# Kernel optimization log

Measured on AMD Instinct MI355X. Metric: run time of the kernel, lower is better.

Reference implementation:

```python
import jax, jax.numpy as jnp
import numpy as np

# ---- model dims (match init_kwargs) ----
B, C, T = 64, 128, 512          # batch, n_channel, n_tokens
H = 256                          # n_hidden
GRID_SIZE = 5
SPLINE_ORDER = 3
N_COEFF = GRID_SIZE + SPLINE_ORDER   # 8 basis functions per input feature
GRID_RANGE = (-1.0, 1.0)
LN_EPS = 1e-5


def make_grid(in_features):
    # efficient-KAN extended knot grid: (in_features, grid_size + 2*order + 1)
    h = (GRID_RANGE[1] - GRID_RANGE[0]) / GRID_SIZE
    g = jnp.arange(-SPLINE_ORDER, GRID_SIZE + SPLINE_ORDER + 1, dtype=jnp.float32) * h + GRID_RANGE[0]
    return jnp.broadcast_to(g, (in_features, g.shape[0]))


def b_splines(x, grid):
    # x: (N, in), grid: (in, G+2k+1) -> (N, in, G+k) via Cox-de Boor recursion
    xg = x[:, :, None]
    bases = ((xg >= grid[:, :-1]) & (xg < grid[:, 1:])).astype(x.dtype)
    for k in range(1, SPLINE_ORDER + 1):
        left = (xg - grid[:, : -(k + 1)]) / (grid[:, k:-1] - grid[:, : -(k + 1)])
        right = (grid[:, k + 1:] - xg) / (grid[:, k + 1:] - grid[:, 1:-k])
        bases = left * bases[:, :, :-1] + right * bases[:, :, 1:]
    return bases


def kan_linear(x, grid, base_w, spline_w, spline_scaler):
    # x: (..., in) -> (..., out). base: silu(x)@W^T, plus spline combination.
    lead = x.shape[:-1]
    x2 = x.reshape(-1, x.shape[-1])
    base_out = jax.nn.silu(x2) @ base_w.T                              # (N, out)
    sw = spline_w * spline_scaler[:, :, None]                          # (out, in, coeff)
    spl_out = jnp.einsum('nic,oic->no', b_splines(x2, grid), sw)       # (N, out)
    return (base_out + spl_out).reshape(*lead, base_w.shape[0])


def setup_inputs() -> dict:
    key = jax.random.key(0)
    ks = jax.random.split(key, 8)
    scale1 = 1.0 / np.sqrt(C)
    scale2 = 1.0 / np.sqrt(H)
    return {
        "U": jax.random.normal(ks[0], (B, C, T), dtype=jnp.float32),
        "ln_w": jnp.ones((T, C), dtype=jnp.float32),
        "ln_b": jnp.zeros((T, C), dtype=jnp.float32),
        "bw1": jax.random.normal(ks[1], (H, C), dtype=jnp.float32) * scale1,
        "sw1": jax.random.normal(ks[2], (H, C, N_COEFF), dtype=jnp.float32) * (0.1 * scale1),
        "ss1": jnp.ones((H, C), dtype=jnp.float32),
        "bw2": jax.random.normal(ks[3], (C, H), dtype=jnp.float32) * scale2,
        "sw2": jax.random.normal(ks[4], (C, H, N_COEFF), dtype=jnp.float32) * (0.1 * scale2),
        "ss2": jnp.ones((C, H), dtype=jnp.float32),
    }


def reference(U, ln_w, ln_b, bw1, sw1, ss1, bw2, sw2, ss2):
    g1 = make_grid(C)
    g2 = make_grid(H)
    z = jnp.transpose(U, (0, 2, 1))                                   # (B, T, C)
    mu = jnp.mean(z, axis=(-2, -1), keepdims=True)
    var = jnp.var(z, axis=(-2, -1), keepdims=True)
    z = (z - mu) * jax.lax.rsqrt(var + LN_EPS) * ln_w + ln_b          # LN over [T, C]
    z = kan_linear(z, g1, bw1, sw1, ss1)                              # (B, T, H)
    z = kan_linear(z, g2, bw2, sw2, ss2)                              # (B, T, C)
    return U + jnp.transpose(z, (0, 2, 1))
```

## Files before the change

kernel.cpp:

```cpp
#include <hip/hip_runtime.h>
#include <math.h>

namespace {

constexpr int Bn = 64, Cn = 128, Tn = 512, Hn = 256;
constexpr int MR = 32;
constexpr int TB = Tn / MR;
constexpr int K1 = Cn * 9;
constexpr int K2 = Hn * 9;
constexpr int FC = 16;
constexpr int KC = 144;
constexpr int KSS = 152;
constexpr int HS = 274;
constexpr int NCH1 = 8, NCH2 = 16;
constexpr float LN_EPS = 1e-5f;

typedef __attribute__((ext_vector_type(8))) short short8;
typedef __attribute__((ext_vector_type(16))) float f32x16;

__device__ __forceinline__ unsigned short f2bf(float f) {
  unsigned int u = __builtin_bit_cast(unsigned int, f);
  u = (u + 0x7fffu + ((u >> 16) & 1u)) >> 16;
  return (unsigned short)u;
}
__device__ __forceinline__ float bf2f(unsigned short u) {
  unsigned int v = (unsigned int)u << 16;
  return __builtin_bit_cast(float, v);
}

__device__ __forceinline__ void act_store(float z,
                                          unsigned short* __restrict__ rowp,
                                          int feat) {
  const float e = __expf(-z);
  rowp[128 + feat] = f2bf(z * __builtin_amdgcn_rcpf(1.0f + e));
  const float p = z * 2.5f + 5.5f;
  const float fi = floorf(p);
  const int ib = (int)fi - 3;
  const float u = p - fi;
  const float u2 = u * u, u3 = u2 * u, tt = 1.0f - u;
  const float wv0 = tt * tt * tt * (1.0f / 6.0f);
  const float wv1 = (3.0f * u3 - 6.0f * u2 + 4.0f) * (1.0f / 6.0f);
  const float wv2 = (-3.0f * u3 + 3.0f * u2 + 3.0f * u + 1.0f) * (1.0f / 6.0f);
  const float wv3 = u3 * (1.0f / 6.0f);
  const float wv[4] = {wv0, wv1, wv2, wv3};
#pragma unroll
  for (int s = 0; s < 4; ++s) {
    const int j = ib + s;
    const int off = (j >= 0 && j <= 7) ? j * 16 + feat : 144 + (feat & 7);
    rowp[off] = f2bf(wv[s]);
  }
}

}

__global__ __launch_bounds__(256) void kan_prep(
    const float* __restrict__ U, const float* __restrict__ ln_w,
    const float* __restrict__ ln_b, const float* __restrict__ bw1,
    const float* __restrict__ sw1, const float* __restrict__ ss1,
    const float* __restrict__ bw2, const float* __restrict__ sw2,
    const float* __restrict__ ss2, unsigned short* __restrict__ W1p,
    unsigned short* __restrict__ W2p, unsigned short* __restrict__ lnwT,
    unsigned short* __restrict__ lnbT, float* __restrict__ stats) {
  __shared__ float red[2][4];
  const int blk = blockIdx.x;
  if (blk < 256) {
    int idx = blk * 256 + threadIdx.x;
    if (idx < Hn * Cn) {
      const int h = idx >> 7, c = idx & 127;
      const float* spw = sw1 + ((size_t)h * Cn + c) * 8;
      const float sc = ss1[h * Cn + c];
      unsigned short* dst = W1p + (size_t)h * K1 + (c >> 4) * KC + (c & 15);
#pragma unroll
      for (int j = 0; j < 8; ++j) dst[j * 16] = f2bf(spw[j] * sc);
      dst[8 * 16] = f2bf(bw1[h * Cn + c]);
    } else {
      idx -= Hn * Cn;
      const int c = idx >> 8, h = idx & 255;
      const float* spw = sw2 + ((size_t)c * Hn + h) * 8;
      const float sc = ss2[c * Hn + h];
      unsigned short* dst = W2p + (size_t)c * K2 + (h >> 4) * KC + (h & 15);
#pragma unroll
      for (int j = 0; j < 8; ++j) dst[j * 16] = f2bf(spw[j] * sc);
      dst[8 * 16] = f2bf(bw2[c * Hn + h]);
    }
  } else if (blk < 512) {
    const int sblk = blk - 256;
    const int b = sblk >> 2, q = sblk & 3;
    const float4* p =
        (const float4*)(U + (size_t)b * (Cn * Tn) + q * (Cn * Tn / 4));
    float s = 0.f, s2 = 0.f;
#pragma unroll 4
    for (int i = threadIdx.x; i < (Cn * Tn / 4) / 4; i += 256) {
      const float4 v = p[i];
      s += v.x + v.y + v.z + v.w;
      s2 += v.x * v.x + v.y * v.y + v.z * v.z + v.w * v.w;
    }
#pragma unroll
    for (int off = 32; off > 0; off >>= 1) {
      s += __shfl_down(s, off);
      s2 += __shfl_down(s2, off);
    }
    if ((threadIdx.x & 63) == 0) {
      red[0][threadIdx.x >> 6] = s;
      red[1][threadIdx.x >> 6] = s2;
    }
    __syncthreads();
    if (threadIdx.x == 0) {
      stats[b * 8 + q * 2 + 0] = red[0][0] + red[0][1] + red[0][2] + red[0][3];
      stats[b * 8 + q * 2 + 1] = red[1][0] + red[1][1] + red[1][2] + red[1][3];
    }
  } else {
    const int bb = blk - 512;
    const float* src = (bb < 64) ? ln_w : ln_b;
    unsigned short* dst = (bb < 64) ? lnwT : lnbT;
    const int base = (bb & 63) * 1024;
#pragma unroll
    for (int e2 = 0; e2 < 4; ++e2) {
      const int i = base + (int)threadIdx.x + e2 * 256;
      const int c = i >> 9, t = i & 511;
      dst[i] = f2bf(src[t * Cn + c]);
    }
  }
}

__global__ __launch_bounds__(512, 4) void kan_fused(
    const float* __restrict__ U, const unsigned short* __restrict__ lnwT,
    const unsigned short* __restrict__ lnbT,
    const unsigned short* __restrict__ W1p,
    const unsigned short* __restrict__ W2p, const float* __restrict__ stats,
    float* __restrict__ out) {
  __shared__ unsigned short s_buf[2][MR * KSS];
  __shared__ unsigned short s_h1[MR * HS];

  const int tid = threadIdx.x;
  const int b = blockIdx.x >> 4;
  const int t0 = (blockIdx.x & 15) * MR;

  const float* sp = stats + b * 8;
  const float ssum = sp[0] + sp[2] + sp[4] + sp[6];
  const float ssq = sp[1] + sp[3] + sp[5] + sp[7];
  const float inv_n = 1.0f / (float)(Cn * Tn);
  const float mean = ssum * inv_n;
  const float rstd = rsqrtf(ssq * inv_n - mean * mean + LN_EPS);

  const int w = tid >> 6, l = tid & 63;
  const int ln31 = l & 31, hl = l >> 5;
  const int a_feat = tid >> 5;
  const int a_row = tid & 31;

  auto zero1 = [&](unsigned short* nbuf) {
    unsigned int* zb = (unsigned int*)nbuf;
#pragma unroll
    for (int it = 0; it < 4; ++it) {
      const int e = l + it * 64;
      zb[(e & 31) * (KSS / 2) + (e >> 5) * 8 + w] = 0u;
    }
  };
  auto zero2 = [&](unsigned short* nbuf) {
    unsigned int* zb = (unsigned int*)nbuf;
#pragma unroll
    for (int it = 0; it < 8; ++it) {
      const int e = l + it * 64;
      const int idx = e >> 5;
      zb[(e & 31) * (KSS / 2) + (idx >> 1) * 8 + 2 * w + (idx & 1)] = 0u;
    }
  };

  auto act1_load = [&](int chunk, float& uS, unsigned short& wS,
                       unsigned short& bS) {
    const int c = chunk * FC + a_feat;
    const int t = t0 + a_row;
    uS = U[((size_t)b * Cn + c) * Tn + t];
    wS = lnwT[c * Tn + t];
    bS = lnbT[c * Tn + t];
  };
  auto act1_fire = [&](unsigned short* nbuf, float uS, unsigned short wS,
                       unsigned short bS) {
    zero1(nbuf);
    const float z = (uS - mean) * rstd * bf2f(wS) + bf2f(bS);
    act_store(z, nbuf + a_row * KSS, a_feat);
  };
  auto act2_all = [&](int chunk, unsigned short* nbuf) {
    zero2(nbuf);
    const int pf = tid >> 4;
#pragma unroll
    for (int pp = 0; pp < 2; ++pp) {
      const int row = (l & 15) + pp * 16;
      const float z = bf2f(s_h1[row * HS + chunk * FC + pf]);
      act_store(z, nbuf + row * KSS, pf);
    }
  };

  short8 breg0[9], breg1[9];
  const unsigned short* wb1 = W1p + (size_t)(w * 32 + ln31) * K1 + hl * 8;
#pragma unroll
  for (int ks = 0; ks < 9; ++ks) breg0[ks] = *(const short8*)(wb1 + ks * 16);
  {
    float uS;
    unsigned short wS, bS;
    act1_load(0, uS, wS, bS);
    act1_fire(s_buf[0], uS, wS, bS);
  }
  __syncthreads();

  f32x16 acc1 = {};
  auto l1step = [&](int kk, const unsigned short* CUR, unsigned short* NXT,
                    short8(&BC)[9], short8(&BN)[9]) {
    const bool more = kk < NCH1 - 1;
    float uS = 0.f;
    unsigned short wS = 0, bS = 0;
    if (more) {
#pragma unroll
      for (int ks = 0; ks < 9; ++ks)
        BN[ks] = *(const short8*)(wb1 + (kk + 1) * KC + ks * 16);
      act1_load(kk + 1, uS, wS, bS);
    }
    __builtin_amdgcn_sched_barrier(0);
    const unsigned short* ap = CUR + ln31 * KSS + hl * 8;
#pragma unroll
    for (int ks = 0; ks < 9; ++ks) {
      const short8 a = *(const short8*)(ap + ks * 16);
      acc1 = __builtin_amdgcn_mfma_f32_32x32x16_bf16(a, BC[ks], acc1, 0, 0, 0);
    }
    if (more) act1_fire(NXT, uS, wS, bS);
    __syncthreads();
  };
  for (int k = 0; k < NCH1; k += 2) {
    l1step(k, s_buf[0], s_buf[1], breg0, breg1);
    l1step(k + 1, s_buf[1], s_buf[0], breg1, breg0);
  }

  const unsigned short* wb2 = W2p + (size_t)((w & 3) * 32 + ln31) * K2 + hl * 8;
  if (w >= 4) {
#pragma unroll
    for (int ks = 0; ks < 9; ++ks) breg0[ks] = *(const short8*)(wb2 + ks * 16);
  }
#pragma unroll
  for (int r = 0; r < 16; ++r) {
    const int row = 4 * hl + (r & 3) + 8 * (r >> 2);
    s_h1[row * HS + w * 32 + ln31] = f2bf(acc1[r]);
  }
  __syncthreads();
  if (w < 4) act2_all(0, s_buf[0]);
  __syncthreads();

  f32x16 acc2 = {};
  auto l2step = [&](int kk, const unsigned short* CUR, unsigned short* NXT,
                    short8(&BC)[9], short8(&BN)[9]) {
    const bool more = kk < NCH2 - 1;
    if (w >= 4) {
      if (more) {
#pragma unroll
        for (int ks = 0; ks < 9; ++ks)
          BN[ks] = *(const short8*)(wb2 + (kk + 1) * KC + ks * 16);
      }
      __builtin_amdgcn_sched_barrier(0);
      const unsigned short* ap = CUR + ln31 * KSS + hl * 8;
      __builtin_amdgcn_s_setprio(1);
#pragma unroll
      for (int ks = 0; ks < 9; ++ks) {
        const short8 a = *(const short8*)(ap + ks * 16);
        acc2 =
            __builtin_amdgcn_mfma_f32_32x32x16_bf16(a, BC[ks], acc2, 0, 0, 0);
      }
      __builtin_amdgcn_s_setprio(0);
    } else {
      if (more) act2_all(kk + 1, NXT);
    }
    __syncthreads();
  };
  for (int k = 0; k < NCH2; k += 2) {
    l2step(k, s_buf[0], s_buf[1], breg0, breg1);
    l2step(k + 1, s_buf[1], s_buf[0], breg1, breg0);
  }

  if (w >= 4) {
    const int c = (w & 3) * 32 + ln31;
#pragma unroll
    for (int g = 0; g < 4; ++g) {
      const int tb = t0 + 4 * hl + 8 * g;
      const size_t base = ((size_t)b * Cn + c) * Tn + tb;
      const float4 uin = *(const float4*)(U + base);
      float4 o;
      o.x = uin.x + acc2[g * 4 + 0];
      o.y = uin.y + acc2[g * 4 + 1];
      o.z = uin.z + acc2[g * 4 + 2];
      o.w = uin.w + acc2[g * 4 + 3];
      *(float4*)(out + base) = o;
    }
  }
}

extern "C" void kernel_launch(void* const* d_in, const int* in_sizes, int n_in,
                              void* d_out, int out_size, void* d_ws,
                              size_t ws_size, hipStream_t stream) {
  const float* U = (const float*)d_in[0];
  const float* ln_w = (const float*)d_in[1];
  const float* ln_b = (const float*)d_in[2];
  const float* bw1 = (const float*)d_in[3];
  const float* sw1 = (const float*)d_in[4];
  const float* ss1 = (const float*)d_in[5];
  const float* bw2 = (const float*)d_in[6];
  const float* sw2 = (const float*)d_in[7];
  const float* ss2 = (const float*)d_in[8];
  float* out = (float*)d_out;

  char* ws = (char*)d_ws;
  float* stats = (float*)ws;
  unsigned short* lnwT = (unsigned short*)(ws + 4096);
  unsigned short* lnbT = lnwT + Cn * Tn;
  unsigned short* W1p = lnbT + Cn * Tn;
  unsigned short* W2p = W1p + (size_t)Hn * K1;

  kan_prep<<<640, 256, 0, stream>>>(U, ln_w, ln_b, bw1, sw1, ss1, bw2, sw2,
                                    ss2, W1p, W2p, lnwT, lnbT, stats);
  kan_fused<<<Bn * TB, 512, 0, stream>>>(U, lnwT, lnbT, W1p, W2p, stats, out);
}
```

Measured before the change: 151.3 us.

## Enlarge row tile to 128 and stream swizzled weights into LDS via direct loads

Result: slower. 176.9 us (+16.9%).

```diff
diff --git a/kernel.cpp b/kernel.cpp
--- a/kernel.cpp
+++ b/kernel.cpp
@@ -4,16 +4,15 @@
 namespace {
 
 constexpr int Bn = 64, Cn = 128, Tn = 512, Hn = 256;
-constexpr int MR = 32;
+constexpr int MR = 128;
 constexpr int TB = Tn / MR;
-constexpr int K1 = Cn * 9;
-constexpr int K2 = Hn * 9;
-constexpr int FC = 16;
-constexpr int KC = 144;
-constexpr int KSS = 152;
-constexpr int HS = 274;
-constexpr int NCH1 = 8, NCH2 = 16;
 constexpr float LN_EPS = 1e-5f;
+
+constexpr int NQ = 54;
+constexpr int RB = 144;
+constexpr int L1B = 36864;
+constexpr int L2B = 18432;
+constexpr int W2OFF = 18 * L1B;
 
 typedef __attribute__((ext_vector_type(8))) short short8;
 typedef __attribute__((ext_vector_type(16))) float f32x16;
@@ -27,62 +26,88 @@
   unsigned int v = (unsigned int)u << 16;
   return __builtin_bit_cast(float, v);
 }
-
-__device__ __forceinline__ void act_store(float z,
-                                          unsigned short* __restrict__ rowp,
-                                          int feat) {
-  const float e = __expf(-z);
-  rowp[128 + feat] = f2bf(z * __builtin_amdgcn_rcpf(1.0f + e));
+__device__ __forceinline__ float siluf(float z) {
+  return z * __builtin_amdgcn_rcpf(1.0f + __expf(-z));
+}
+
+__device__ __forceinline__ short8 spline_pack(float z) {
   const float p = z * 2.5f + 5.5f;
   const float fi = floorf(p);
   const int ib = (int)fi - 3;
   const float u = p - fi;
   const float u2 = u * u, u3 = u2 * u, tt = 1.0f - u;
-  const float wv0 = tt * tt * tt * (1.0f / 6.0f);
-  const float wv1 = (3.0f * u3 - 6.0f * u2 + 4.0f) * (1.0f / 6.0f);
-  const float wv2 = (-3.0f * u3 + 3.0f * u2 + 3.0f * u + 1.0f) * (1.0f / 6.0f);
-  const float wv3 = u3 * (1.0f / 6.0f);
-  const float wv[4] = {wv0, wv1, wv2, wv3};
-#pragma unroll
-  for (int s = 0; s < 4; ++s) {
-    const int j = ib + s;
-    const int off = (j >= 0 && j <= 7) ? j * 16 + feat : 144 + (feat & 7);
-    rowp[off] = f2bf(wv[s]);
-  }
-}
-
-}
+  const float w0 = tt * tt * tt * (1.0f / 6.0f);
+  const float w1 = (3.0f * u3 - 6.0f * u2 + 4.0f) * (1.0f / 6.0f);
+  const float w2 = (-3.0f * u3 + 3.0f * u2 + 3.0f * u + 1.0f) * (1.0f / 6.0f);
+  const float w3 = u3 * (1.0f / 6.0f);
+  short8 r;
+#pragma unroll
+  for (int j = 0; j < 8; ++j) {
+    const int d = j - ib;
+    const float v =
+        (d == 0) ? w0 : (d == 1) ? w1 : (d == 2) ? w2 : (d == 3) ? w3 : 0.0f;
+    r[j] = (short)f2bf(v);
+  }
+  return r;
+}
+
+__device__ __forceinline__ size_t wsrc_byte(int q) {
+  return (q < 18) ? (size_t)q * L1B : (size_t)W2OFF + (size_t)(q - 18) * L2B;
+}
+
+}
+
+#define BAR_LGKM()                                         \
+  do {                                                     \
+    asm volatile("s_waitcnt lgkmcnt(0)" ::: "memory");     \
+    __builtin_amdgcn_s_barrier();                          \
+    asm volatile("" ::: "memory");                         \
+  } while (0)
+#define BAR_FULL()                                                  \
+  do {                                                              \
+    asm volatile("s_waitcnt vmcnt(0) lgkmcnt(0)" ::: "memory");     \
+    __builtin_amdgcn_s_barrier();                                   \
+    asm volatile("" ::: "memory");                                  \
+  } while (0)
 
 __global__ __launch_bounds__(256) void kan_prep(
     const float* __restrict__ U, const float* __restrict__ ln_w,
     const float* __restrict__ ln_b, const float* __restrict__ bw1,
     const float* __restrict__ sw1, const float* __restrict__ ss1,
     const float* __restrict__ bw2, const float* __restrict__ sw2,
-    const float* __restrict__ ss2, unsigned short* __restrict__ W1p,
-    unsigned short* __restrict__ W2p, unsigned short* __restrict__ lnwT,
-    unsigned short* __restrict__ lnbT, float* __restrict__ stats) {
+    const float* __restrict__ ss2, unsigned short* __restrict__ Wp,
+    unsigned short* __restrict__ lnwT, unsigned short* __restrict__ lnbT,
+    float* __restrict__ stats) {
   __shared__ float red[2][4];
   const int blk = blockIdx.x;
-  if (blk < 256) {
-    int idx = blk * 256 + threadIdx.x;
-    if (idx < Hn * Cn) {
-      const int h = idx >> 7, c = idx & 127;
-      const float* spw = sw1 + ((size_t)h * Cn + c) * 8;
-      const float sc = ss1[h * Cn + c];
-      unsigned short* dst = W1p + (size_t)h * K1 + (c >> 4) * KC + (c & 15);
-#pragma unroll
-      for (int j = 0; j < 8; ++j) dst[j * 16] = f2bf(spw[j] * sc);
-      dst[8 * 16] = f2bf(bw1[h * Cn + c]);
-    } else {
-      idx -= Hn * Cn;
-      const int c = idx >> 8, h = idx & 255;
-      const float* spw = sw2 + ((size_t)c * Hn + h) * 8;
-      const float sc = ss2[c * Hn + h];
-      unsigned short* dst = W2p + (size_t)c * K2 + (h >> 4) * KC + (h & 15);
-#pragma unroll
-      for (int j = 0; j < 8; ++j) dst[j * 16] = f2bf(spw[j] * sc);
-      dst[8 * 16] = f2bf(bw2[c * Hn + h]);
-    }
+  if (blk < 128) {
+    const int idx = blk * 256 + threadIdx.x;
+    const int h = idx >> 7, c = idx & 127;
+    const float sc = ss1[idx];
+    const float* spw = sw1 + (size_t)idx * 8;
+    const int swz = ((h >> 3) & 3) << 4;
+    short8 v;
+#pragma unroll
+    for (int j = 0; j < 8; ++j) v[j] = (short)f2bf(spw[j] * sc);
+    const int sb = (h * RB + (c & 7) * 16) ^ swz;
+    *(short8*)((char*)Wp + (size_t)(c >> 3) * L1B + sb) = v;
+    const int ub = (h * RB + (c & 63) * 2) ^ swz;
+    *(unsigned short*)((char*)Wp + (size_t)(16 + (c >> 6)) * L1B + ub) =
+        f2bf(bw1[idx]);
+  } else if (blk < 256) {
+    const int idx = (blk - 128) * 256 + threadIdx.x;
+    const int c = idx >> 8, h = idx & 255;
+    const float sc = ss2[idx];
+    const float* spw = sw2 + (size_t)idx * 8;
+    const int swz = ((c >> 3) & 3) << 4;
+    short8 v;
+#pragma unroll
+    for (int j = 0; j < 8; ++j) v[j] = (short)f2bf(spw[j] * sc);
+    const int sb = (c * RB + (h & 7) * 16) ^ swz;
+    *(short8*)((char*)Wp + W2OFF + (size_t)(h >> 3) * L2B + sb) = v;
+    const int ub = (c * RB + (h & 63) * 2) ^ swz;
+    *(unsigned short*)((char*)Wp + W2OFF + (size_t)(32 + (h >> 6)) * L2B + ub) =
+        f2bf(bw2[idx]);
   } else if (blk < 512) {
     const int sblk = blk - 256;
     const int b = sblk >> 2, q = sblk & 3;
@@ -91,9 +116,9 @@
     float s = 0.f, s2 = 0.f;
 #pragma unroll 4
     for (int i = threadIdx.x; i < (Cn * Tn / 4) / 4; i += 256) {
-      const float4 v = p[i];
-      s += v.x + v.y + v.z + v.w;
-      s2 += v.x * v.x + v.y * v.y + v.z * v.z + v.w * v.w;
+      const float4 v4 = p[i];
+      s += v4.x + v4.y + v4.z + v4.w;
+      s2 += v4.x * v4.x + v4.y * v4.y + v4.z * v4.z + v4.w * v4.w;
     }
 #pragma unroll
     for (int off = 32; off > 0; off >>= 1) {
@@ -117,24 +142,23 @@
 #pragma unroll
     for (int e2 = 0; e2 < 4; ++e2) {
       const int i = base + (int)threadIdx.x + e2 * 256;
-      const int c = i >> 9, t = i & 511;
-      dst[i] = f2bf(src[t * Cn + c]);
-    }
-  }
-}
-
-__global__ __launch_bounds__(512, 4) void kan_fused(
+      dst[i] = f2bf(src[(i & 511) * Cn + (i >> 9)]);
+    }
+  }
+}
+
+__global__ __launch_bounds__(512, 2) void kan_fused(
     const float* __restrict__ U, const unsigned short* __restrict__ lnwT,
     const unsigned short* __restrict__ lnbT,
-    const unsigned short* __restrict__ W1p,
-    const unsigned short* __restrict__ W2p, const float* __restrict__ stats,
+    const unsigned short* __restrict__ Wp, const float* __restrict__ stats,
     float* __restrict__ out) {
-  __shared__ unsigned short s_buf[2][MR * KSS];
-  __shared__ unsigned short s_h1[MR * HS];
+  __shared__ __align__(16) unsigned short s_w[2][L1B / 2];
+  __shared__ __align__(16) unsigned short s_a[MR * 72];
+  __shared__ __align__(16) unsigned short s_h1[MR * 258];
 
   const int tid = threadIdx.x;
-  const int b = blockIdx.x >> 4;
-  const int t0 = (blockIdx.x & 15) * MR;
+  const int b = blockIdx.x >> 2;
+  const int t0 = (blockIdx.x & 3) * MR;
 
   const float* sp = stats + b * 8;
   const float ssum = sp[0] + sp[2] + sp[4] + sp[6];
@@ -145,147 +169,263 @@
 
   const int w = tid >> 6, l = tid & 63;
   const int ln31 = l & 31, hl = l >> 5;
-  const int a_feat = tid >> 5;
-  const int a_row = tid & 31;
-
-  auto zero1 = [&](unsigned short* nbuf) {
-    unsigned int* zb = (unsigned int*)nbuf;
-#pragma unroll
-    for (int it = 0; it < 4; ++it) {
-      const int e = l + it * 64;
-      zb[(e & 31) * (KSS / 2) + (e >> 5) * 8 + w] = 0u;
+  const int mi = w >> 2, ni = w & 3;
+  const int arow = tid & 127;
+  const int afe = tid >> 7;
+  const int aswz = ((arow >> 3) & 3) << 4;
+  const int fswz = ((ln31 >> 3) & 3) << 4;
+
+  f32x16 acc00 = {}, acc01 = {}, acc10 = {}, acc11 = {};
+  f32x16 acc20 = {}, acc21 = {};
+
+  auto stage = [&](int q, int buf) {
+    const char* src = (const char*)Wp + wsrc_byte(q);
+    char* dstb = (char*)&s_w[buf][0];
+    const int nIss = (q < 18) ? 36 : 18;
+    for (int i = w; i < nIss; i += 8) {
+      const char* gp = src + i * 1024 + l * 16;
+      char* lp = dstb + i * 1024;
+      __builtin_amdgcn_global_load_lds(
+          (const __attribute__((address_space(1))) unsigned int*)gp,
+          (__attribute__((address_space(3))) unsigned int*)lp, 16, 0, 0);
     }
   };
-  auto zero2 = [&](unsigned short* nbuf) {
-    unsigned int* zb = (unsigned int*)nbuf;
-#pragma unroll
-    for (int it = 0; it < 8; ++it) {
-      const int e = l + it * 64;
-      const int idx = e >> 5;
-      zb[(e & 31) * (KSS / 2) + (idx >> 1) * 8 + 2 * w + (idx & 1)] = 0u;
-    }
+
+  auto store8 = [&](int f, short8 v) {
+    *(short8*)((char*)s_a + ((arow * RB + f * 16) ^ aswz)) = v;
   };
 
-  auto act1_load = [&](int chunk, float& uS, unsigned short& wS,
-                       unsigned short& bS) {
-    const int c = chunk * FC + a_feat;
-    const int t = t0 + a_row;
-    uS = U[((size_t)b * Cn + c) * Tn + t];
-    wS = lnwT[c * Tn + t];
-    bS = lnbT[c * Tn + t];
+  auto mfma_l1 = [&](int buf) {
+    const char* ab = (const char*)s_a;
+    const char* bb = (const char*)&s_w[buf][0];
+    const int ra0 = (mi * 64 + ln31) * RB, ra1 = ra0 + 32 * RB;
+    const int rb0 = (ni * 64 + ln31) * RB, rb1 = rb0 + 32 * RB;
+#pragma unroll
+    for (int ks = 0; ks < 4; ++ks) {
+      const int kb = ks * 32 + hl * 16;
+      const short8 a0 = *(const short8*)(ab + ((ra0 + kb) ^ fswz));
+      const short8 a1 = *(const short8*)(ab + ((ra1 + kb) ^ fswz));
+      const short8 b0 = *(const short8*)(bb + ((rb0 + kb) ^ fswz));
+      const short8 b1 = *(const short8*)(bb + ((rb1 + kb) ^ fswz));
+      acc00 = __builtin_amdgcn_mfma_f32_32x32x16_bf16(a0, b0, acc00, 0, 0, 0);
+      acc01 = __builtin_amdgcn_mfma_f32_32x32x16_bf16(a0, b1, acc01, 0, 0, 0);
+      acc10 = __builtin_amdgcn_mfma_f32_32x32x16_bf16(a1, b0, acc10, 0, 0, 0);
+      acc11 = __builtin_amdgcn_mfma_f32_32x32x16_bf16(a1, b1, acc11, 0, 0, 0);
+    }
   };
-  auto act1_fire = [&](unsigned short* nbuf, float uS, unsigned short wS,
-                       unsigned short bS) {
-    zero1(nbuf);
-    const float z = (uS - mean) * rstd * bf2f(wS) + bf2f(bS);
-    act_store(z, nbuf + a_row * KSS, a_feat);
+  auto mfma_l2 = [&](int buf) {
+    const char* ab = (const char*)s_a;
+    const char* bb = (const char*)&s_w[buf][0];
+    const int ra0 = (mi * 64 + ln31) * RB, ra1 = ra0 + 32 * RB;
+    const int rb0 = (ni * 32 + ln31) * RB;
+#pragma unroll
+    for (int ks = 0; ks < 4; ++ks) {
+      const int kb = ks * 32 + hl * 16;
+      const short8 a0 = *(const short8*)(ab + ((ra0 + kb) ^ fswz));
+      const short8 a1 = *(const short8*)(ab + ((ra1 + kb) ^ fswz));
+      const short8 b0 = *(const short8*)(bb + ((rb0 + kb) ^ fswz));
+      acc20 = __builtin_amdgcn_mfma_f32_32x32x16_bf16(a0, b0, acc20, 0, 0, 0);
+      acc21 = __builtin_amdgcn_mfma_f32_32x32x16_bf16(a1, b0, acc21, 0, 0, 0);
+    }
   };
-  auto act2_all = [&](int chunk, unsigned short* nbuf) {
-    zero2(nbuf);
-    const int pf = tid >> 4;
-#pragma unroll
-    for (int pp = 0; pp < 2; ++pp) {
-      const int row = (l & 15) + pp * 16;
-      const float z = bf2f(s_h1[row * HS + chunk * FC + pf]);
-      act_store(z, nbuf + row * KSS, pf);
-    }
-  };
-
-  short8 breg0[9], breg1[9];
-  const unsigned short* wb1 = W1p + (size_t)(w * 32 + ln31) * K1 + hl * 8;
-#pragma unroll
-  for (int ks = 0; ks < 9; ++ks) breg0[ks] = *(const short8*)(wb1 + ks * 16);
+
   {
-    float uS;
-    unsigned short wS, bS;
-    act1_load(0, uS, wS, bS);
-    act1_fire(s_buf[0], uS, wS, bS);
-  }
-  __syncthreads();
-
-  f32x16 acc1 = {};
-  auto l1step = [&](int kk, const unsigned short* CUR, unsigned short* NXT,
-                    short8(&BC)[9], short8(&BN)[9]) {
-    const bool more = kk < NCH1 - 1;
-    float uS = 0.f;
-    unsigned short wS = 0, bS = 0;
+    const int t = t0 + arow;
+    const int c0 = afe, c1 = afe + 4;
+    const float zu0 = U[((size_t)b * Cn + c0) * Tn + t];
+    const float zu1 = U[((size_t)b * Cn + c1) * Tn + t];
+    const unsigned short w0 = lnwT[c0 * Tn + t], b0 = lnbT[c0 * Tn + t];
+    const unsigned short w1 = lnwT[c1 * Tn + t], b1 = lnbT[c1 * Tn + t];
+    stage(0, 0);
+    const float z0 = (zu0 - mean) * rstd * bf2f(w0) + bf2f(b0);
+    const float z1 = (zu1 - mean) * rstd * bf2f(w1) + bf2f(b1);
+    store8(afe, spline_pack(z0));
+    store8(afe + 4, spline_pack(z1));
+  }
+  BAR_FULL();
+
+  for (int q = 0; q < 16; ++q) {
+    const int buf = q & 1;
+    float zu0 = 0.f, zu1 = 0.f;
+    unsigned short w0 = 0, w1 = 0, b0 = 0, b1 = 0;
+    float pf0[8], pf1[8];
+    unsigned short pu0[8], pu1[8], pv0[8], pv1[8];
+    const bool nspl = q < 15;
+    {
+      const int t = t0 + arow;
+      if (nspl) {
+        const int c0 = (q + 1) * 8 + afe, c1 = c0 + 4;
+        zu0 = U[((size_t)b * Cn + c0) * Tn + t];
+        zu1 = U[((size_t)b * Cn + c1) * Tn + t];
+        w0 = lnwT[c0 * Tn + t]; b0 = lnbT[c0 * Tn + t];
+        w1 = lnwT[c1 * Tn + t]; b1 = lnbT[c1 * Tn + t];
+      } else {
+#pragma unroll
+        for (int j = 0; j < 8; ++j) {
+          const int c0 = afe * 8 + j, c1 = (afe + 4) * 8 + j;
+          pf0[j] = U[((size_t)b * Cn + c0) * Tn + t];
+          pu0[j] = lnwT[c0 * Tn + t]; pv0[j] = lnbT[c0 * Tn + t];
+          pf1[j] = U[((size_t)b * Cn + c1) * Tn + t];
+          pu1[j] = lnwT[c1 * Tn + t]; pv1[j] = lnbT[c1 * Tn + t];
+        }
+      }
+      stage(q + 1, buf ^ 1);
+      mfma_l1(buf);
+    }
+    BAR_LGKM();
+    {
+      if (nspl) {
+        const float z0 = (zu0 - mean) * rstd * bf2f(w0) + bf2f(b0);
+        const float z1 = (zu1 - mean) * rstd * bf2f(w1) + bf2f(b1);
+        store8(afe, spline_pack(z0));
+        store8(afe + 4, spline_pack(z1));
+      } else {
+        short8 va, vb;
+#pragma unroll
+        for (int j = 0; j < 8; ++j) {
+          va[j] = (short)f2bf(
+              siluf((pf0[j] - mean) * rstd * bf2f(pu0[j]) + bf2f(pv0[j])));
+          vb[j] = (short)f2bf(
+              siluf((pf1[j] - mean) * rstd * bf2f(pu1[j]) + bf2f(pv1[j])));
+        }
+        store8(afe, va);
+        store8(afe + 4, vb);
+      }
+    }
+    BAR_FULL();
+  }
+
+  {
+    float pf0[8], pf1[8];
+    unsigned short pu0[8], pu1[8], pv0[8], pv1[8];
+    const int t = t0 + arow;
+#pragma unroll
+    for (int j = 0; j < 8; ++j) {
+      const int c0 = 64 + afe * 8 + j, c1 = 64 + (afe + 4) * 8 + j;
+      pf0[j] = U[((size_t)b * Cn + c0) * Tn + t];
+      pu0[j] = lnwT[c0 * Tn + t]; pv0[j] = lnbT[c0 * Tn + t];
+      pf1[j] = U[((size_t)b * Cn + c1) * Tn + t];
+      pu1[j] = lnwT[c1 * Tn + t]; pv1[j] = lnbT[c1 * Tn + t];
+    }
+    stage(17, 1);
+    mfma_l1(0);
+    BAR_LGKM();
+    short8 va, vb;
+#pragma unroll
+    for (int j = 0; j < 8; ++j) {
+      va[j] = (short)f2bf(
+          siluf((pf0[j] - mean) * rstd * bf2f(pu0[j]) + bf2f(pv0[j])));
+      vb[j] = (short)f2bf(
+          siluf((pf1[j] - mean) * rstd * bf2f(pu1[j]) + bf2f(pv1[j])));
+    }
+    store8(afe, va);
+    store8(afe + 4, vb);
+    BAR_FULL();
+  }
+  {
+    stage(18, 0);
+    mfma_l1(1);
+    BAR_LGKM();
+#pragma unroll
+    for (int r = 0; r < 16; ++r) {
+      const int rr = 4 * hl + (r & 3) + 8 * (r >> 2);
+      const int colb = ni * 64 + ln31;
+      s_h1[(mi * 64 + rr) * 258 + colb] = f2bf(acc00[r]);
+      s_h1[(mi * 64 + rr) * 258 + colb + 32] = f2bf(acc01[r]);
+      s_h1[(mi * 64 + 32 + rr) * 258 + colb] = f2bf(acc10[r]);
+      s_h1[(mi * 64 + 32 + rr) * 258 + colb + 32] = f2bf(acc11[r]);
+    }
+    BAR_LGKM();
+    const float z0 = bf2f(s_h1[arow * 258 + afe]);
+    const float z1 = bf2f(s_h1[arow * 258 + afe + 4]);
+    store8(afe, spline_pack(z0));
+    store8(afe + 4, spline_pack(z1));
+    BAR_FULL();
+  }
+
+  for (int q = 18; q < 50; ++q) {
+    const int buf = q & 1;
+    unsigned short h0 = 0, h1v = 0;
+    unsigned short pu0[8], pu1[8];
+    const bool nspl = q < 49;
+    {
+      if (nspl) {
+        const int hb = (q - 17) * 8;
+        h0 = s_h1[arow * 258 + hb + afe];
+        h1v = s_h1[arow * 258 + hb + afe + 4];
+      } else {
+#pragma unroll
+        for (int j = 0; j < 8; ++j) {
+          pu0[j] = s_h1[arow * 258 + afe * 8 + j];
+          pu1[j] = s_h1[arow * 258 + (afe + 4) * 8 + j];
+        }
+      }
+      stage(q + 1, buf ^ 1);
+      mfma_l2(buf);
+    }
+    BAR_LGKM();
+    {
+      if (nspl) {
+        store8(afe, spline_pack(bf2f(h0)));
+        store8(afe + 4, spline_pack(bf2f(h1v)));
+      } else {
+        short8 va, vb;
+#pragma unroll
+        for (int j = 0; j < 8; ++j) {
+          va[j] = (short)f2bf(siluf(bf2f(pu0[j])));
+          vb[j] = (short)f2bf(siluf(bf2f(pu1[j])));
+        }
+        store8(afe, va);
+        store8(afe + 4, vb);
+      }
+    }
+    BAR_FULL();
+  }
+
+  for (int q = 50; q < NQ; ++q) {
+    const int buf = q & 1;
+    unsigned short pu0[8], pu1[8];
+    const bool more = q < NQ - 1;
+    {
+      if (more) {
+        const int hb = (q - 49) * 64;
+#pragma unroll
+        for (int j = 0; j < 8; ++j) {
+          pu0[j] = s_h1[arow * 258 + hb + afe * 8 + j];
+          pu1[j] = s_h1[arow * 258 + hb + (afe + 4) * 8 + j];
+        }
+        stage(q + 1, buf ^ 1);
+      }
+      mfma_l2(buf);
+    }
     if (more) {
-#pragma unroll
-      for (int ks = 0; ks < 9; ++ks)
-        BN[ks] = *(const short8*)(wb1 + (kk + 1) * KC + ks * 16);
-      act1_load(kk + 1, uS, wS, bS);
-    }
-    __builtin_amdgcn_sched_barrier(0);
-    const unsigned short* ap = CUR + ln31 * KSS + hl * 8;
-#pragma unroll
-    for (int ks = 0; ks < 9; ++ks) {
-      const short8 a = *(const short8*)(ap + ks * 16);
-      acc1 = __builtin_amdgcn_mfma_f32_32x32x16_bf16(a, BC[ks], acc1, 0, 0, 0);
-    }
-    if (more) act1_fire(NXT, uS, wS, bS);
-    __syncthreads();
-  };
-  for (int k = 0; k < NCH1; k += 2) {
-    l1step(k, s_buf[0], s_buf[1], breg0, breg1);
-    l1step(k + 1, s_buf[1], s_buf[0], breg1, breg0);
-  }
-
-  const unsigned short* wb2 = W2p + (size_t)((w & 3) * 32 + ln31) * K2 + hl * 8;
-  if (w >= 4) {
-#pragma unroll
-    for (int ks = 0; ks < 9; ++ks) breg0[ks] = *(const short8*)(wb2 + ks * 16);
-  }
-#pragma unroll
-  for (int r = 0; r < 16; ++r) {
-    const int row = 4 * hl + (r & 3) + 8 * (r >> 2);
-    s_h1[row * HS + w * 32 + ln31] = f2bf(acc1[r]);
-  }
-  __syncthreads();
-  if (w < 4) act2_all(0, s_buf[0]);
-  __syncthreads();
-
-  f32x16 acc2 = {};
-  auto l2step = [&](int kk, const unsigned short* CUR, unsigned short* NXT,
-                    short8(&BC)[9], short8(&BN)[9]) {
-    const bool more = kk < NCH2 - 1;
-    if (w >= 4) {
-      if (more) {
-#pragma unroll
-        for (int ks = 0; ks < 9; ++ks)
-          BN[ks] = *(const short8*)(wb2 + (kk + 1) * KC + ks * 16);
-      }
-      __builtin_amdgcn_sched_barrier(0);
-      const unsigned short* ap = CUR + ln31 * KSS + hl * 8;
-      __builtin_amdgcn_s_setprio(1);
-#pragma unroll
-      for (int ks = 0; ks < 9; ++ks) {
-        const short8 a = *(const short8*)(ap + ks * 16);
-        acc2 =
-            __builtin_amdgcn_mfma_f32_32x32x16_bf16(a, BC[ks], acc2, 0, 0, 0);
-      }
-      __builtin_amdgcn_s_setprio(0);
-    } else {
-      if (more) act2_all(kk + 1, NXT);
-    }
-    __syncthreads();
-  };
-  for (int k = 0; k < NCH2; k += 2) {
-    l2step(k, s_buf[0], s_buf[1], breg0, breg1);
-    l2step(k + 1, s_buf[1], s_buf[0], breg1, breg0);
-  }
-
-  if (w >= 4) {
-    const int c = (w & 3) * 32 + ln31;
+      BAR_LGKM();
+      short8 va, vb;
+#pragma unroll
+      for (int j = 0; j < 8; ++j) {
+        va[j] = (short)f2bf(siluf(bf2f(pu0[j])));
+        vb[j] = (short)f2bf(siluf(bf2f(pu1[j])));
+      }
+      store8(afe, va);
+      store8(afe + 4, vb);
+      BAR_FULL();
+    }
+  }
+
+  const int c = ni * 32 + ln31;
+#pragma unroll
+  for (int mi2 = 0; mi2 < 2; ++mi2) {
 #pragma unroll
     for (int g = 0; g < 4; ++g) {
-      const int tb = t0 + 4 * hl + 8 * g;
-      const size_t base = ((size_t)b * Cn + c) * Tn + tb;
+      const int trow = t0 + mi * 64 + mi2 * 32 + 8 * g + 4 * hl;
+      const size_t base = ((size_t)b * Cn + c) * Tn + trow;
       const float4 uin = *(const float4*)(U + base);
       float4 o;
-      o.x = uin.x + acc2[g * 4 + 0];
-      o.y = uin.y + acc2[g * 4 + 1];
-      o.z = uin.z + acc2[g * 4 + 2];
-      o.w = uin.w + acc2[g * 4 + 3];
+      const f32x16& a2 = mi2 ? acc21 : acc20;
+      o.x = uin.x + a2[g * 4 + 0];
+      o.y = uin.y + a2[g * 4 + 1];
+      o.z = uin.z + a2[g * 4 + 2];
+      o.w = uin.w + a2[g * 4 + 3];
       *(float4*)(out + base) = o;
     }
   }
@@ -309,10 +449,9 @@
   float* stats = (float*)ws;
   unsigned short* lnwT = (unsigned short*)(ws + 4096);
   unsigned short* lnbT = lnwT + Cn * Tn;
-  unsigned short* W1p = lnbT + Cn * Tn;
-  unsigned short* W2p = W1p + (size_t)Hn * K1;
+  unsigned short* Wp = lnbT + Cn * Tn;
 
   kan_prep<<<640, 256, 0, stream>>>(U, ln_w, ln_b, bw1, sw1, ss1, bw2, sw2,
-                                    ss2, W1p, W2p, lnwT, lnbT, stats);
-  kan_fused<<<Bn * TB, 512, 0, stream>>>(U, lnwT, lnbT, W1p, W2p, stats, out);
-}
+                                    ss2, Wp, lnwT, lnbT, stats);
+  kan_fused<<<Bn * TB, 512, 0, stream>>>(U, lnwT, lnbT, Wp, stats, out);
+}
```

## Enlarge token tile and stream packed weights into LDS via direct global-to-LDS loads

Applied to the files above, without the earlier changes.

Measured after the change: 254.9 us. +68.4%, slower.

```diff
diff --git a/kernel.cpp b/kernel.cpp
--- a/kernel.cpp
+++ b/kernel.cpp
@@ -4,16 +4,14 @@
 namespace {
 
 constexpr int Bn = 64, Cn = 128, Tn = 512, Hn = 256;
-constexpr int MR = 32;
+constexpr int MR = 128;
 constexpr int TB = Tn / MR;
-constexpr int K1 = Cn * 9;
-constexpr int K2 = Hn * 9;
-constexpr int FC = 16;
-constexpr int KC = 144;
-constexpr int KSS = 152;
-constexpr int HS = 274;
-constexpr int NCH1 = 8, NCH2 = 16;
 constexpr float LN_EPS = 1e-5f;
+
+constexpr int C1 = 16384;
+constexpr int C2 = 8192;
+constexpr int W2S = 18 * C1;
+constexpr int SST = 266;
 
 typedef __attribute__((ext_vector_type(8))) short short8;
 typedef __attribute__((ext_vector_type(16))) float f32x16;
@@ -27,28 +25,29 @@
   unsigned int v = (unsigned int)u << 16;
   return __builtin_bit_cast(float, v);
 }
-
-__device__ __forceinline__ void act_store(float z,
-                                          unsigned short* __restrict__ rowp,
-                                          int feat) {
-  const float e = __expf(-z);
-  rowp[128 + feat] = f2bf(z * __builtin_amdgcn_rcpf(1.0f + e));
+__device__ __forceinline__ float siluf(float z) {
+  return z * __builtin_amdgcn_rcpf(1.0f + __expf(-z));
+}
+
+__device__ __forceinline__ short8 spline_pack(float z) {
   const float p = z * 2.5f + 5.5f;
   const float fi = floorf(p);
   const int ib = (int)fi - 3;
   const float u = p - fi;
   const float u2 = u * u, u3 = u2 * u, tt = 1.0f - u;
-  const float wv0 = tt * tt * tt * (1.0f / 6.0f);
-  const float wv1 = (3.0f * u3 - 6.0f * u2 + 4.0f) * (1.0f / 6.0f);
-  const float wv2 = (-3.0f * u3 + 3.0f * u2 + 3.0f * u + 1.0f) * (1.0f / 6.0f);
-  const float wv3 = u3 * (1.0f / 6.0f);
-  const float wv[4] = {wv0, wv1, wv2, wv3};
-#pragma unroll
-  for (int s = 0; s < 4; ++s) {
-    const int j = ib + s;
-    const int off = (j >= 0 && j <= 7) ? j * 16 + feat : 144 + (feat & 7);
-    rowp[off] = f2bf(wv[s]);
-  }
+  const float w0 = tt * tt * tt * (1.0f / 6.0f);
+  const float w1 = (3.0f * u3 - 6.0f * u2 + 4.0f) * (1.0f / 6.0f);
+  const float w2 = (-3.0f * u3 + 3.0f * u2 + 3.0f * u + 1.0f) * (1.0f / 6.0f);
+  const float w3 = u3 * (1.0f / 6.0f);
+  short8 r;
+#pragma unroll
+  for (int j = 0; j < 8; ++j) {
+    const int d = j - ib;
+    const float v =
+        (d == 0) ? w0 : (d == 1) ? w1 : (d == 2) ? w2 : (d == 3) ? w3 : 0.0f;
+    r[j] = (short)f2bf(v);
+  }
+  return r;
 }
 
 }
@@ -58,31 +57,33 @@
     const float* __restrict__ ln_b, const float* __restrict__ bw1,
     const float* __restrict__ sw1, const float* __restrict__ ss1,
     const float* __restrict__ bw2, const float* __restrict__ sw2,
-    const float* __restrict__ ss2, unsigned short* __restrict__ W1p,
-    unsigned short* __restrict__ W2p, unsigned short* __restrict__ lnwT,
-    unsigned short* __restrict__ lnbT, float* __restrict__ stats) {
+    const float* __restrict__ ss2, unsigned short* __restrict__ Wp,
+    unsigned short* __restrict__ lnwT, unsigned short* __restrict__ lnbT,
+    float* __restrict__ stats) {
   __shared__ float red[2][4];
   const int blk = blockIdx.x;
-  if (blk < 256) {
-    int idx = blk * 256 + threadIdx.x;
-    if (idx < Hn * Cn) {
-      const int h = idx >> 7, c = idx & 127;
-      const float* spw = sw1 + ((size_t)h * Cn + c) * 8;
-      const float sc = ss1[h * Cn + c];
-      unsigned short* dst = W1p + (size_t)h * K1 + (c >> 4) * KC + (c & 15);
-#pragma unroll
-      for (int j = 0; j < 8; ++j) dst[j * 16] = f2bf(spw[j] * sc);
-      dst[8 * 16] = f2bf(bw1[h * Cn + c]);
-    } else {
-      idx -= Hn * Cn;
-      const int c = idx >> 8, h = idx & 255;
-      const float* spw = sw2 + ((size_t)c * Hn + h) * 8;
-      const float sc = ss2[c * Hn + h];
-      unsigned short* dst = W2p + (size_t)c * K2 + (h >> 4) * KC + (h & 15);
-#pragma unroll
-      for (int j = 0; j < 8; ++j) dst[j * 16] = f2bf(spw[j] * sc);
-      dst[8 * 16] = f2bf(bw2[c * Hn + h]);
-    }
+  if (blk < 128) {
+    const int idx = blk * 256 + threadIdx.x;
+    const int h = idx >> 7, c = idx & 127;
+    const float sc = ss1[idx];
+    const float* spw = sw1 + (size_t)idx * 8;
+    short8 v;
+#pragma unroll
+    for (int j = 0; j < 8; ++j) v[j] = (short)f2bf(spw[j] * sc);
+    *(short8*)(Wp + (size_t)(c >> 3) * C1 + ((c & 7) * 256 + h) * 8) = v;
+    Wp[(size_t)(16 + (c >> 6)) * C1 + (((c >> 3) & 7) * 256 + h) * 8 +
+       (c & 7)] = f2bf(bw1[idx]);
+  } else if (blk < 256) {
+    const int idx = (blk - 128) * 256 + threadIdx.x;
+    const int c = idx >> 8, h = idx & 255;
+    const float sc = ss2[idx];
+    const float* spw = sw2 + (size_t)idx * 8;
+    short8 v;
+#pragma unroll
+    for (int j = 0; j < 8; ++j) v[j] = (short)f2bf(spw[j] * sc);
+    *(short8*)(Wp + W2S + (size_t)(h >> 3) * C2 + ((h & 7) * 128 + c) * 8) = v;
+    Wp[W2S + (size_t)(32 + (h >> 6)) * C2 + (((h >> 3) & 7) * 128 + c) * 8 +
+       (h & 7)] = f2bf(bw2[idx]);
   } else if (blk < 512) {
     const int sblk = blk - 256;
     const int b = sblk >> 2, q = sblk & 3;
@@ -91,9 +92,9 @@
     float s = 0.f, s2 = 0.f;
 #pragma unroll 4
     for (int i = threadIdx.x; i < (Cn * Tn / 4) / 4; i += 256) {
-      const float4 v = p[i];
-      s += v.x + v.y + v.z + v.w;
-      s2 += v.x * v.x + v.y * v.y + v.z * v.z + v.w * v.w;
+      const float4 v4 = p[i];
+      s += v4.x + v4.y + v4.z + v4.w;
+      s2 += v4.x * v4.x + v4.y * v4.y + v4.z * v4.z + v4.w * v4.w;
     }
 #pragma unroll
     for (int off = 32; off > 0; off >>= 1) {
@@ -117,24 +118,22 @@
 #pragma unroll
     for (int e2 = 0; e2 < 4; ++e2) {
       const int i = base + (int)threadIdx.x + e2 * 256;
-      const int c = i >> 9, t = i & 511;
-      dst[i] = f2bf(src[t * Cn + c]);
-    }
-  }
-}
-
-__global__ __launch_bounds__(512, 4) void kan_fused(
+      dst[i] = f2bf(src[(i & 511) * Cn + (i >> 9)]);
+    }
+  }
+}
+
+__global__ __launch_bounds__(256, 1) void kan_fused(
     const float* __restrict__ U, const unsigned short* __restrict__ lnwT,
     const unsigned short* __restrict__ lnbT,
-    const unsigned short* __restrict__ W1p,
-    const unsigned short* __restrict__ W2p, const float* __restrict__ stats,
+    const unsigned short* __restrict__ Wp, const float* __restrict__ stats,
     float* __restrict__ out) {
-  __shared__ unsigned short s_buf[2][MR * KSS];
-  __shared__ unsigned short s_h1[MR * HS];
+  __shared__ __align__(16) unsigned short s_b[2][C1];
+  __shared__ __align__(16) unsigned short s_stash[4][32 * SST];
 
   const int tid = threadIdx.x;
-  const int b = blockIdx.x >> 4;
-  const int t0 = (blockIdx.x & 15) * MR;
+  const int b = blockIdx.x >> 2;
+  const int t0 = (blockIdx.x & 3) * MR;
 
   const float* sp = stats + b * 8;
   const float ssum = sp[0] + sp[2] + sp[4] + sp[6];
@@ -145,149 +144,122 @@
 
   const int w = tid >> 6, l = tid & 63;
   const int ln31 = l & 31, hl = l >> 5;
-  const int a_feat = tid >> 5;
-  const int a_row = tid & 31;
-
-  auto zero1 = [&](unsigned short* nbuf) {
-    unsigned int* zb = (unsigned int*)nbuf;
-#pragma unroll
-    for (int it = 0; it < 4; ++it) {
-      const int e = l + it * 64;
-      zb[(e & 31) * (KSS / 2) + (e >> 5) * 8 + w] = 0u;
+  const int trow = t0 + w * 32 + ln31;
+  unsigned short* stash = s_stash[w];
+
+  auto stage = [&](int q, int buf) {
+    const char* src =
+        (const char*)Wp + ((q < 18) ? (size_t)q * 32768
+                                    : (size_t)589824 + (size_t)(q - 18) * 16384);
+    char* dst = (char*)&s_b[buf][0];
+    const int n = (q < 18) ? 32 : 16;
+    for (int i = w; i < n; i += 4) {
+      __builtin_amdgcn_global_load_lds(
+          (const __attribute__((address_space(1))) unsigned int*)(src +
+                                                                  i * 1024 +
+                                                                  l * 16),
+          (__attribute__((address_space(3))) unsigned int*)(dst + i * 1024),
+          16, 0, 0);
     }
   };
-  auto zero2 = [&](unsigned short* nbuf) {
-    unsigned int* zb = (unsigned int*)nbuf;
-#pragma unroll
-    for (int it = 0; it < 8; ++it) {
-      const int e = l + it * 64;
-      const int idx = e >> 5;
-      zb[(e & 31) * (KSS / 2) + (idx >> 1) * 8 + 2 * w + (idx & 1)] = 0u;
-    }
-  };
-
-  auto act1_load = [&](int chunk, float& uS, unsigned short& wS,
-                       unsigned short& bS) {
-    const int c = chunk * FC + a_feat;
-    const int t = t0 + a_row;
-    uS = U[((size_t)b * Cn + c) * Tn + t];
-    wS = lnwT[c * Tn + t];
-    bS = lnbT[c * Tn + t];
-  };
-  auto act1_fire = [&](unsigned short* nbuf, float uS, unsigned short wS,
-                       unsigned short bS) {
-    zero1(nbuf);
-    const float z = (uS - mean) * rstd * bf2f(wS) + bf2f(bS);
-    act_store(z, nbuf + a_row * KSS, a_feat);
-  };
-  auto act2_all = [&](int chunk, unsigned short* nbuf) {
-    zero2(nbuf);
-    const int pf = tid >> 4;
-#pragma unroll
-    for (int pp = 0; pp < 2; ++pp) {
-      const int row = (l & 15) + pp * 16;
-      const float z = bf2f(s_h1[row * HS + chunk * FC + pf]);
-      act_store(z, nbuf + row * KSS, pf);
-    }
-  };
-
-  short8 breg0[9], breg1[9];
-  const unsigned short* wb1 = W1p + (size_t)(w * 32 + ln31) * K1 + hl * 8;
-#pragma unroll
-  for (int ks = 0; ks < 9; ++ks) breg0[ks] = *(const short8*)(wb1 + ks * 16);
-  {
-    float uS;
-    unsigned short wS, bS;
-    act1_load(0, uS, wS, bS);
-    act1_fire(s_buf[0], uS, wS, bS);
-  }
+
+  f32x16 acc1[8] = {};
+  stage(0, 0);
   __syncthreads();
-
-  f32x16 acc1 = {};
-  auto l1step = [&](int kk, const unsigned short* CUR, unsigned short* NXT,
-                    short8(&BC)[9], short8(&BN)[9]) {
-    const bool more = kk < NCH1 - 1;
-    float uS = 0.f;
-    unsigned short wS = 0, bS = 0;
-    if (more) {
-#pragma unroll
-      for (int ks = 0; ks < 9; ++ks)
-        BN[ks] = *(const short8*)(wb1 + (kk + 1) * KC + ks * 16);
-      act1_load(kk + 1, uS, wS, bS);
-    }
-    __builtin_amdgcn_sched_barrier(0);
-    const unsigned short* ap = CUR + ln31 * KSS + hl * 8;
-#pragma unroll
-    for (int ks = 0; ks < 9; ++ks) {
-      const short8 a = *(const short8*)(ap + ks * 16);
-      acc1 = __builtin_amdgcn_mfma_f32_32x32x16_bf16(a, BC[ks], acc1, 0, 0, 0);
-    }
-    if (more) act1_fire(NXT, uS, wS, bS);
+  for (int q = 0; q < 18; ++q) {
+    const int buf = q & 1;
+    stage(q + 1, buf ^ 1);
+    const unsigned short* bb = &s_b[buf][0];
+#pragma unroll
+    for (int ks = 0; ks < 4; ++ks) {
+      short8 a;
+      if (q < 16) {
+        const int c = q * 8 + ks * 2 + hl;
+        const float uv = U[((size_t)b * Cn + c) * Tn + trow];
+        const float z = (uv - mean) * rstd * bf2f(lnwT[c * Tn + trow]) +
+                        bf2f(lnbT[c * Tn + trow]);
+        stash[ln31 * SST + c] = f2bf(z);
+        a = spline_pack(z);
+      } else {
+        const int cb = (q - 16) * 64 + ks * 16 + hl * 8;
+        const short8 zs = *(const short8*)&stash[ln31 * SST + cb];
+#pragma unroll
+        for (int j = 0; j < 8; ++j)
+          a[j] = (short)f2bf(siluf(bf2f((unsigned short)zs[j])));
+      }
+      const unsigned short* fb = bb + ((ks * 2 + hl) * 256 + ln31) * 8;
+#pragma unroll
+      for (int nt = 0; nt < 8; ++nt) {
+        const short8 bfr = *(const short8*)(fb + nt * 256);
+        acc1[nt] =
+            __builtin_amdgcn_mfma_f32_32x32x16_bf16(a, bfr, acc1[nt], 0, 0, 0);
+      }
+    }
     __syncthreads();
-  };
-  for (int k = 0; k < NCH1; k += 2) {
-    l1step(k, s_buf[0], s_buf[1], breg0, breg1);
-    l1step(k + 1, s_buf[1], s_buf[0], breg1, breg0);
-  }
-
-  const unsigned short* wb2 = W2p + (size_t)((w & 3) * 32 + ln31) * K2 + hl * 8;
-  if (w >= 4) {
-#pragma unroll
-    for (int ks = 0; ks < 9; ++ks) breg0[ks] = *(const short8*)(wb2 + ks * 16);
-  }
-#pragma unroll
-  for (int r = 0; r < 16; ++r) {
-    const int row = 4 * hl + (r & 3) + 8 * (r >> 2);
-    s_h1[row * HS + w * 32 + ln31] = f2bf(acc1[r]);
-  }
+  }
+
+#pragma unroll
+  for (int nt = 0; nt < 8; ++nt)
+#pragma unroll
+    for (int r = 0; r < 16; ++r) {
+      const int row = 4 * hl + (r & 3) + 8 * (r >> 2);
+      stash[row * SST + nt * 32 + ln31] = f2bf(acc1[nt][r]);
+    }
+
+  f32x16 acc2[4] = {};
+  for (int q = 18; q < 54; ++q) {
+    const int buf = q & 1;
+    if (q < 53) stage(q + 1, buf ^ 1);
+    const unsigned short* bb = &s_b[buf][0];
+#pragma unroll
+    for (int ks = 0; ks < 4; ++ks) {
+      short8 a;
+      if (q < 50) {
+        const int h = (q - 18) * 8 + ks * 2 + hl;
+        a = spline_pack(bf2f(stash[ln31 * SST + h]));
+      } else {
+        const int hb = (q - 50) * 64 + ks * 16 + hl * 8;
+        const short8 zs = *(const short8*)&stash[ln31 * SST + hb];
+#pragma unroll
+        for (int j = 0; j < 8; ++j)
+          a[j] = (short)f2bf(siluf(bf2f((unsigned short)zs[j])));
+      }
+      const unsigned short* fb = bb + ((ks * 2 + hl) * 128 + ln31) * 8;
+#pragma unroll
+      for (int nt = 0; nt < 4; ++nt) {
+        const short8 bfr = *(const short8*)(fb + nt * 256);
+        acc2[nt] =
+            __builtin_amdgcn_mfma_f32_32x32x16_bf16(a, bfr, acc2[nt], 0, 0, 0);
+      }
+    }
+    __syncthreads();
+  }
+
+  float* ob = (float*)&s_b[0][0];
+#pragma unroll
+  for (int nt = 0; nt < 4; ++nt)
+#pragma unroll
+    for (int r = 0; r < 16; ++r) {
+      const int c = nt * 32 + ln31;
+      const int row = 4 * hl + (r & 3) + 8 * (r >> 2);
+      ob[w * 4096 + c * 32 + (row ^ ((c & 7) << 2))] = acc2[nt][r];
+    }
   __syncthreads();
-  if (w < 4) act2_all(0, s_buf[0]);
-  __syncthreads();
-
-  f32x16 acc2 = {};
-  auto l2step = [&](int kk, const unsigned short* CUR, unsigned short* NXT,
-                    short8(&BC)[9], short8(&BN)[9]) {
-    const bool more = kk < NCH2 - 1;
-    if (w >= 4) {
-      if (more) {
-#pragma unroll
-        for (int ks = 0; ks < 9; ++ks)
-          BN[ks] = *(const short8*)(wb2 + (kk + 1) * KC + ks * 16);
-      }
-      __builtin_amdgcn_sched_barrier(0);
-      const unsigned short* ap = CUR + ln31 * KSS + hl * 8;
-      __builtin_amdgcn_s_setprio(1);
-#pragma unroll
-      for (int ks = 0; ks < 9; ++ks) {
-        const short8 a = *(const short8*)(ap + ks * 16);
-        acc2 =
-            __builtin_amdgcn_mfma_f32_32x32x16_bf16(a, BC[ks], acc2, 0, 0, 0);
-      }
-      __builtin_amdgcn_s_setprio(0);
-    } else {
-      if (more) act2_all(kk + 1, NXT);
-    }
-    __syncthreads();
-  };
-  for (int k = 0; k < NCH2; k += 2) {
-    l2step(k, s_buf[0], s_buf[1], breg0, breg1);
-    l2step(k + 1, s_buf[1], s_buf[0], breg1, breg0);
-  }
-
-  if (w >= 4) {
-    const int c = (w & 3) * 32 + ln31;
-#pragma unroll
-    for (int g = 0; g < 4; ++g) {
-      const int tb = t0 + 4 * hl + 8 * g;
-      const size_t base = ((size_t)b * Cn + c) * Tn + tb;
-      const float4 uin = *(const float4*)(U + base);
-      float4 o;
-      o.x = uin.x + acc2[g * 4 + 0];
-      o.y = uin.y + acc2[g * 4 + 1];
-      o.z = uin.z + acc2[g * 4 + 2];
-      o.w = uin.w + acc2[g * 4 + 3];
-      *(float4*)(out + base) = o;
-    }
+#pragma unroll 4
+  for (int it = 0; it < 16; ++it) {
+    const int slot = it * 256 + tid;
+    const int ws = slot >> 10, rem = slot & 1023;
+    const int c = rem >> 3, rg = rem & 7;
+    const int p4 = (rg * 4) ^ ((c & 7) << 2);
+    const float4 v = *(const float4*)&ob[ws * 4096 + c * 32 + p4];
+    const size_t ga = ((size_t)b * Cn + c) * Tn + t0 + ws * 32 + rg * 4;
+    const float4 u4 = *(const float4*)&U[ga];
+    float4 o;
+    o.x = u4.x + v.x;
+    o.y = u4.y + v.y;
+    o.z = u4.z + v.z;
+    o.w = u4.w + v.w;
+    *(float4*)&out[ga] = o;
   }
 }
 
@@ -309,10 +281,9 @@
   float* stats = (float*)ws;
   unsigned short* lnwT = (unsigned short*)(ws + 4096);
   unsigned short* lnbT = lnwT + Cn * Tn;
-  unsigned short* W1p = lnbT + Cn * Tn;
-  unsigned short* W2p = W1p + (size_t)Hn * K1;
+  unsigned short* Wp = lnbT + Cn * Tn;
 
   kan_prep<<<640, 256, 0, stream>>>(U, ln_w, ln_b, bw1, sw1, ss1, bw2, sw2,
-                                    ss2, W1p, W2p, lnwT, lnbT, stats);
-  kan_fused<<<Bn * TB, 512, 0, stream>>>(U, lnwT, lnbT, W1p, W2p, stats, out);
-}
+                                    ss2, Wp, lnwT, lnbT, stats);
+  kan_fused<<<Bn * TB, 256, 0, stream>>>(U, lnwT, lnbT, Wp, stats, out);
+}
```
